# Kernel optimization log

Hardware: AMD Instinct MI355X
Metric: run time of the kernel (lower is better)

The kernel has to match this reference:

```python
import jax, jax.numpy as jnp
import numpy as np

B, T, D, H, HD, L, V = 2048, 64, 128, 4, 32, 6, 256
DFF = 4 * D
PARAM_NAMES = ['tok_emb', 'pos_emb', 'Wq', 'Wk', 'Wv', 'Wo', 'bo', 'ln1_g', 'ln1_b',
               'W1', 'b1', 'W2', 'b2', 'ln2_g', 'ln2_b', 'lnf_g', 'lnf_b', 'Wh', 'bh']


def setup_inputs() -> dict:
    key = jax.random.key(0)
    ks = jax.random.split(key, 12)
    def n(k, shape, s=0.02):
        return jax.random.normal(k, shape, jnp.float32) * s
    return dict(
        idx=jax.random.randint(ks[0], (B, T), 0, V),
        tok_emb=n(ks[1], (V, D)),
        pos_emb=n(ks[2], (T, D)),
        Wq=n(ks[3], (L, H, D, HD)),
        Wk=n(ks[4], (L, H, D, HD)),
        Wv=n(ks[5], (L, H, D, HD)),
        Wo=n(ks[6], (L, D, D)), bo=jnp.zeros((L, D), jnp.float32),
        ln1_g=jnp.ones((L, D), jnp.float32), ln1_b=jnp.zeros((L, D), jnp.float32),
        W1=n(ks[7], (L, D, DFF)), b1=jnp.zeros((L, DFF), jnp.float32),
        W2=n(ks[8], (L, DFF, D)), b2=jnp.zeros((L, D), jnp.float32),
        ln2_g=jnp.ones((L, D), jnp.float32), ln2_b=jnp.zeros((L, D), jnp.float32),
        lnf_g=jnp.ones((D,), jnp.float32), lnf_b=jnp.zeros((D,), jnp.float32),
        Wh=n(ks[9], (D, V)), bh=jnp.zeros((V,), jnp.float32),
    )


def _ln(x, g, b):
    m = x.mean(-1, keepdims=True)
    v = x.var(-1, keepdims=True)  # biased, matches torch LayerNorm
    return (x - m) / jnp.sqrt(v + 1e-5) * g + b


def _forward(idx, p):
    x = p['tok_emb'][idx] + p['pos_emb'][None, :, :]  # [B,T,D]
    mask = jnp.tril(jnp.ones((T, T), bool))

    def block(x, lp):
        Wq, Wk, Wv, Wo, bo, g1, bb1, W1, b1, W2, b2, g2, bb2 = lp
        h = _ln(x, g1, bb1)
        q = jnp.einsum('btd,hde->bhte', h, Wq)
        k = jnp.einsum('btd,hde->bhte', h, Wk)
        v = jnp.einsum('btd,hde->bhte', h, Wv)
        s = jnp.einsum('bhte,bhse->bhts', q, k) * (HD ** -0.5)
        s = jnp.where(mask, s, -jnp.inf)
        w = jax.nn.softmax(s, axis=-1)  # dropout inactive (eval mode)
        o = jnp.einsum('bhts,bhse->bthe', w, v).reshape(B, T, D)  # concat heads
        x = x + o @ Wo + bo
        h2 = _ln(x, g2, bb2)
        x = x + jax.nn.relu(h2 @ W1 + b1) @ W2 + b2
        return x, None

    lp = (p['Wq'], p['Wk'], p['Wv'], p['Wo'], p['bo'], p['ln1_g'], p['ln1_b'],
          p['W1'], p['b1'], p['W2'], p['b2'], p['ln2_g'], p['ln2_b'])
    x, _ = jax.lax.scan(block, x, lp)
    x = _ln(x, p['lnf_g'], p['lnf_b'])
    return x @ p['Wh'] + p['bh']  # [B,T,V] logits


def reference(idx, tok_emb, pos_emb, Wq, Wk, Wv, Wo, bo, ln1_g, ln1_b,
              W1, b1, W2, b2, ln2_g, ln2_b, lnf_g, lnf_b, Wh, bh):
    p = dict(zip(PARAM_NAMES, (tok_emb, pos_emb, Wq, Wk, Wv, Wo, bo, ln1_g, ln1_b,
                               W1, b1, W2, b2, ln2_g, ln2_b, lnf_g, lnf_b, Wh, bh)))
    return _forward(idx, p)
```

## Files before the change

kernel.cpp:

```cpp
#include <hip/hip_runtime.h>

typedef unsigned short ushort_t;
typedef __attribute__((ext_vector_type(8))) short short8;
typedef __attribute__((ext_vector_type(4))) float float4_;

#define B_   2048
#define T_   64
#define D_   128
#define H_   4
#define HD_  32
#define L_   6
#define V_   256
#define DFF_ 512
#define BT_  (B_*T_)

static __device__ __forceinline__ float b2f(ushort_t u) {
    return __uint_as_float(((unsigned int)u) << 16);
}
static __device__ __forceinline__ ushort_t f2b(float f) {
    unsigned int x = __float_as_uint(f);
    return (ushort_t)((x + 0x7fffu + ((x >> 16) & 1u)) >> 16);
}
static __device__ __forceinline__ int bf16_mode(const ushort_t* flag_src) {
    return flag_src[0] == 0x3F80;
}

#define AS1C(p) ((const __attribute__((address_space(1))) void*)(p))
#define AS3(p)  ((__attribute__((address_space(3))) void*)(p))

#define NCVT 19
struct Cvt {
    const void* src[NCVT];
    long base[NCVT];
    long total;
};

__global__ __launch_bounds__(256) void convert_all(
    Cvt c, ushort_t* __restrict__ dst, const ushort_t* __restrict__ flag_src)
{
    long i = (long)blockIdx.x * 256 + threadIdx.x;
    if (i >= c.total) return;
    int s = 0;
    #pragma unroll 1
    while (s + 1 < NCVT && i >= c.base[s + 1]) s++;
    long j = i - c.base[s];
    if (bf16_mode(flag_src))
        dst[i] = ((const ushort_t*)c.src[s])[j];
    else
        dst[i] = f2b(((const float*)c.src[s])[j]);
}

__global__ __launch_bounds__(256) void repack_qkv(
    const ushort_t* __restrict__ Wq, const ushort_t* __restrict__ Wk,
    const ushort_t* __restrict__ Wv, ushort_t* __restrict__ outw)
{
    int i = blockIdx.x * 256 + threadIdx.x;
    int d = i & 127;
    int c = (i >> 7) % 384;
    int l = i / (384 * 128);
    int sel = c >> 7, hh = (c >> 5) & 3, e = c & 31;
    const ushort_t* W = (sel == 0) ? Wq : (sel == 1) ? Wk : Wv;
    outw[i] = W[((l * 4 + hh) * 128 + d) * 32 + e];
}

__global__ __launch_bounds__(256) void transpose_w(
    const ushort_t* __restrict__ in, ushort_t* __restrict__ out, int K, int N)
{
    long i = (long)blockIdx.x * 256 + threadIdx.x;
    int n = (int)(i % N);
    int k = (int)((i / N) % K);
    int l = (int)(i / ((long)N * K));
    out[((long)l * N + n) * K + k] = in[i];
}

__global__ __launch_bounds__(256) void embed_ln_kernel(
    const int* __restrict__ idx, const ushort_t* __restrict__ tok,
    const ushort_t* __restrict__ pos, const ushort_t* __restrict__ g,
    const ushort_t* __restrict__ bta, float* __restrict__ x,
    ushort_t* __restrict__ hout)
{
    int row  = blockIdx.x * 4 + (threadIdx.x >> 6);
    int lane = threadIdx.x & 63;
    int t = row & 63;
    int id = idx[row];
    float v0 = b2f(tok[id * 128 + lane])      + b2f(pos[t * 128 + lane]);
    float v1 = b2f(tok[id * 128 + lane + 64]) + b2f(pos[t * 128 + lane + 64]);
    long o = (long)row * 128 + lane;
    x[o] = v0; x[o + 64] = v1;
    float s  = v0 + v1;
    float sq = v0 * v0 + v1 * v1;
    #pragma unroll
    for (int off = 1; off < 64; off <<= 1) {
        s  += __shfl_xor(s,  off);
        sq += __shfl_xor(sq, off);
    }
    float mean = s * (1.0f / 128.0f);
    float var  = sq * (1.0f / 128.0f) - mean * mean;
    float rstd = rsqrtf(var + 1e-5f);
    hout[o]      = f2b((v0 - mean) * rstd * b2f(g[lane])      + b2f(bta[lane]));
    hout[o + 64] = f2b((v1 - mean) * rstd * b2f(g[lane + 64]) + b2f(bta[lane + 64]));
}

__global__ __launch_bounds__(256) void gemm_bt(
    const ushort_t* __restrict__ A, const ushort_t* __restrict__ Bt,
    const ushort_t* __restrict__ bias, void* __restrict__ outp,
    const ushort_t* __restrict__ flag, int M, int N, int K, int relu)
{
    __shared__ __align__(16) ushort_t As[128 * 64];
    __shared__ __align__(16) ushort_t Bs[128 * 64];
    const int tid  = threadIdx.x;
    const int wave = tid >> 6, lane = tid & 63;
    const int wm = wave >> 1, wn = wave & 1;
    const int row0 = blockIdx.x * 128, col0 = blockIdx.y * 128;

    float4_ acc[4][4];
    #pragma unroll
    for (int m = 0; m < 4; m++)
        #pragma unroll
        for (int n = 0; n < 4; n++) acc[m][n] = (float4_)0.0f;

    const int srow = lane >> 3;
    const int scg  = (lane & 7) ^ srow;
    const int fr = lane & 15, fq = lane >> 4;

    for (int k0 = 0; k0 < K; k0 += 64) {
        __syncthreads();
        #pragma unroll
        for (int i = 0; i < 4; i++) {
            int chunk = wave * 4 + i;
            int r = chunk * 8 + srow;
            __builtin_amdgcn_global_load_lds(
                AS1C(&A[(size_t)(row0 + r) * K + k0 + scg * 8]),
                AS3(&As[chunk * 512]), 16, 0, 0);
            __builtin_amdgcn_global_load_lds(
                AS1C(&Bt[(size_t)(col0 + r) * K + k0 + scg * 8]),
                AS3(&Bs[chunk * 512]), 16, 0, 0);
        }
        __syncthreads();

        #pragma unroll
        for (int ks = 0; ks < 2; ks++) {
            short8 af[4], bf[4];
            #pragma unroll
            for (int mt = 0; mt < 4; mt++) {
                int r = wm * 64 + mt * 16 + fr;
                af[mt] = *(const short8*)&As[r * 64 + (((ks * 4 + fq) ^ (r & 7)) * 8)];
            }
            #pragma unroll
            for (int nt = 0; nt < 4; nt++) {
                int r = wn * 64 + nt * 16 + fr;
                bf[nt] = *(const short8*)&Bs[r * 64 + (((ks * 4 + fq) ^ (r & 7)) * 8)];
            }
            #pragma unroll
            for (int mt = 0; mt < 4; mt++)
                #pragma unroll
                for (int nt = 0; nt < 4; nt++)
                    acc[mt][nt] = __builtin_amdgcn_mfma_f32_16x16x32_bf16(
                        af[mt], bf[nt], acc[mt][nt], 0, 0, 0);
        }
    }

    const int out_bf16 = (flag == nullptr) || bf16_mode(flag);
    #pragma unroll
    for (int nt = 0; nt < 4; nt++) {
        int gcol = col0 + wn * 64 + nt * 16 + fr;
        float bb = bias ? b2f(bias[gcol]) : 0.0f;
        #pragma unroll
        for (int mt = 0; mt < 4; mt++) {
            #pragma unroll
            for (int i = 0; i < 4; i++) {
                int grow = row0 + wm * 64 + mt * 16 + fq * 4 + i;
                float v = acc[mt][nt][i] + bb;
                if (relu) v = fmaxf(v, 0.0f);
                long off = (long)grow * N + gcol;
                if (out_bf16) ((ushort_t*)outp)[off] = f2b(v);
                else          ((float*)outp)[off] = v;
            }
        }
    }
}

__global__ __launch_bounds__(256) void gemm_ln(
    const ushort_t* __restrict__ A, const ushort_t* __restrict__ Bt,
    const ushort_t* __restrict__ bias, float* __restrict__ x,
    const ushort_t* __restrict__ g, const ushort_t* __restrict__ bta,
    ushort_t* __restrict__ hout, int M, int K)
{
    __shared__ __align__(16) ushort_t As[128 * 64];
    __shared__ __align__(16) ushort_t Bs[128 * 64];
    __shared__ float stats[128][2][2];
    const int tid  = threadIdx.x;
    const int wave = tid >> 6, lane = tid & 63;
    const int wm = wave >> 1, wn = wave & 1;
    const int row0 = blockIdx.x * 128;
    const int N = 128;

    float4_ acc[4][4];
    #pragma unroll
    for (int m = 0; m < 4; m++)
        #pragma unroll
        for (int n = 0; n < 4; n++) acc[m][n] = (float4_)0.0f;

    const int srow = lane >> 3;
    const int scg  = (lane & 7) ^ srow;
    const int fr = lane & 15, fq = lane >> 4;

    for (int k0 = 0; k0 < K; k0 += 64) {
        __syncthreads();
        #pragma unroll
        for (int i = 0; i < 4; i++) {
            int chunk = wave * 4 + i;
            int r = chunk * 8 + srow;
            __builtin_amdgcn_global_load_lds(
                AS1C(&A[(size_t)(row0 + r) * K + k0 + scg * 8]),
                AS3(&As[chunk * 512]), 16, 0, 0);
            __builtin_amdgcn_global_load_lds(
                AS1C(&Bt[(size_t)r * K + k0 + scg * 8]),
                AS3(&Bs[chunk * 512]), 16, 0, 0);
        }
        __syncthreads();

        #pragma unroll
        for (int ks = 0; ks < 2; ks++) {
            short8 af[4], bf[4];
            #pragma unroll
            for (int mt = 0; mt < 4; mt++) {
                int r = wm * 64 + mt * 16 + fr;
                af[mt] = *(const short8*)&As[r * 64 + (((ks * 4 + fq) ^ (r & 7)) * 8)];
            }
            #pragma unroll
            for (int nt = 0; nt < 4; nt++) {
                int r = wn * 64 + nt * 16 + fr;
                bf[nt] = *(const short8*)&Bs[r * 64 + (((ks * 4 + fq) ^ (r & 7)) * 8)];
            }
            #pragma unroll
            for (int mt = 0; mt < 4; mt++)
                #pragma unroll
                for (int nt = 0; nt < 4; nt++)
                    acc[mt][nt] = __builtin_amdgcn_mfma_f32_16x16x32_bf16(
                        af[mt], bf[nt], acc[mt][nt], 0, 0, 0);
        }
    }

    int   col[4];
    float bbias[4], gg[4], bln[4];
    #pragma unroll
    for (int nt = 0; nt < 4; nt++) {
        col[nt]  = wn * 64 + nt * 16 + fr;
        bbias[nt] = b2f(bias[col[nt]]);
        gg[nt]    = b2f(g[col[nt]]);
        bln[nt]   = b2f(bta[col[nt]]);
    }
    #pragma unroll
    for (int mt = 0; mt < 4; mt++) {
        #pragma unroll
        for (int i = 0; i < 4; i++) {
            int lr = wm * 64 + mt * 16 + fq * 4 + i;
            long rbase = (long)(row0 + lr) * N;
            float s = 0.0f, sq = 0.0f;
            #pragma unroll
            for (int nt = 0; nt < 4; nt++) {
                float nx = x[rbase + col[nt]] + acc[mt][nt][i] + bbias[nt];
                x[rbase + col[nt]] = nx;
                acc[mt][nt][i] = nx;
                s += nx; sq += nx * nx;
            }
            s  += __shfl_xor(s, 1);  sq += __shfl_xor(sq, 1);
            s  += __shfl_xor(s, 2);  sq += __shfl_xor(sq, 2);
            s  += __shfl_xor(s, 4);  sq += __shfl_xor(sq, 4);
            s  += __shfl_xor(s, 8);  sq += __shfl_xor(sq, 8);
            if (fr == 0) { stats[lr][wn][0] = s; stats[lr][wn][1] = sq; }
        }
    }
    __syncthreads();
    #pragma unroll
    for (int mt = 0; mt < 4; mt++) {
        #pragma unroll
        for (int i = 0; i < 4; i++) {
            int lr = wm * 64 + mt * 16 + fq * 4 + i;
            float s  = stats[lr][0][0] + stats[lr][1][0];
            float sq = stats[lr][0][1] + stats[lr][1][1];
            float mean = s * (1.0f / 128.0f);
            float var  = sq * (1.0f / 128.0f) - mean * mean;
            float rstd = rsqrtf(var + 1e-5f);
            long rbase = (long)(row0 + lr) * N;
            #pragma unroll
            for (int nt = 0; nt < 4; nt++) {
                float nx = acc[mt][nt][i];
                hout[rbase + col[nt]] = f2b((nx - mean) * rstd * gg[nt] + bln[nt]);
            }
        }
    }
}

__global__ __launch_bounds__(256) void ffn_fused(
    const ushort_t* __restrict__ hin,
    const ushort_t* __restrict__ w1,
    const ushort_t* __restrict__ b1v,
    const ushort_t* __restrict__ w2,
    const ushort_t* __restrict__ b2v,
    float* __restrict__ x,
    const ushort_t* __restrict__ g, const ushort_t* __restrict__ bta,
    ushort_t* __restrict__ hout)
{
    __shared__ __align__(16) ushort_t Hs[64 * 128];
    __shared__ __align__(16) ushort_t Ms[64 * 128];
    __shared__ __align__(16) ushort_t Bs[128 * 64];
    __shared__ float stats[64][2][2];
    const int tid  = threadIdx.x;
    const int wave = tid >> 6, lane = tid & 63;
    const int wm = wave >> 1, wn = wave & 1;
    const int row0 = blockIdx.x * 64;

    const int srow = lane >> 3;
    const int scg  = (lane & 7) ^ srow;
    const int fr = lane & 15, fq = lane >> 4;

    {
        int lr4 = lane >> 4, pg = lane & 15;
        #pragma unroll
        for (int i = 0; i < 4; i++) {
            int c = wave * 4 + i;
            int r = c * 4 + lr4;
            int kg = pg ^ (r & 7);
            __builtin_amdgcn_global_load_lds(
                AS1C(&hin[(size_t)(row0 + r) * 128 + kg * 8]),
                AS3(&Hs[c * 512]), 16, 0, 0);
        }
    }

    float4_ acc2[2][4];
    #pragma unroll
    for (int m = 0; m < 2; m++)
        #pragma unroll
        for (int n = 0; n < 4; n++) acc2[m][n] = (float4_)0.0f;

    #pragma unroll 1
    for (int c = 0; c < 4; c++) {
        const ushort_t* Wc = w1 + (size_t)c * 128 * 128;
        float4_ acc1[2][4];
        #pragma unroll
        for (int m = 0; m < 2; m++)
            #pragma unroll
            for (int n = 0; n < 4; n++) acc1[m][n] = (float4_)0.0f;

        #pragma unroll 1
        for (int k0 = 0; k0 < 128; k0 += 64) {
            __syncthreads();
            #pragma unroll
            for (int i = 0; i < 4; i++) {
                int chunk = wave * 4 + i;
                int r = chunk * 8 + srow;
                __builtin_amdgcn_global_load_lds(
                    AS1C(&Wc[(size_t)r * 128 + k0 + scg * 8]),
                    AS3(&Bs[chunk * 512]), 16, 0, 0);
            }
            __syncthreads();
            #pragma unroll
            for (int ks = 0; ks < 2; ks++) {
                int kb = (k0 >> 5) + ks;
                short8 af[2], bf[4];
                #pragma unroll
                for (int mt = 0; mt < 2; mt++) {
                    int r = wm * 32 + mt * 16 + fr;
                    af[mt] = *(const short8*)&Hs[r * 128 + (((kb * 4 + fq) ^ (r & 7)) * 8)];
                }
                #pragma unroll
                for (int nt = 0; nt < 4; nt++) {
                    int r = wn * 64 + nt * 16 + fr;
                    bf[nt] = *(const short8*)&Bs[r * 64 + (((ks * 4 + fq) ^ (r & 7)) * 8)];
                }
                #pragma unroll
                for (int mt = 0; mt < 2; mt++)
                    #pragma unroll
                    for (int nt = 0; nt < 4; nt++)
                        acc1[mt][nt] = __builtin_amdgcn_mfma_f32_16x16x32_bf16(
                            af[mt], bf[nt], acc1[mt][nt], 0, 0, 0);
            }
        }

        #pragma unroll
        for (int nt = 0; nt < 4; nt++) {
            int col = wn * 64 + nt * 16 + fr;
            float bb = b2f(b1v[c * 128 + col]);
            #pragma unroll
            for (int mt = 0; mt < 2; mt++) {
                #pragma unroll
                for (int i = 0; i < 4; i++) {
                    int row = wm * 32 + mt * 16 + fq * 4 + i;
                    float v = fmaxf(acc1[mt][nt][i] + bb, 0.0f);
                    Ms[row * 128 + (((col >> 3) ^ (row & 7)) * 8) + (col & 7)] = f2b(v);
                }
            }
        }

        #pragma unroll 1
        for (int k0 = 0; k0 < 128; k0 += 64) {
            __syncthreads();
            #pragma unroll
            for (int i = 0; i < 4; i++) {
                int chunk = wave * 4 + i;
                int r = chunk * 8 + srow;
                __builtin_amdgcn_global_load_lds(
                    AS1C(&w2[(size_t)r * 512 + c * 128 + k0 + scg * 8]),
                    AS3(&Bs[chunk * 512]), 16, 0, 0);
            }
            __syncthreads();
            #pragma unroll
            for (int ks = 0; ks < 2; ks++) {
                int kb = (k0 >> 5) + ks;
                short8 af[2], bf[4];
                #pragma unroll
                for (int mt = 0; mt < 2; mt++) {
                    int r = wm * 32 + mt * 16 + fr;
                    af[mt] = *(const short8*)&Ms[r * 128 + (((kb * 4 + fq) ^ (r & 7)) * 8)];
                }
                #pragma unroll
                for (int nt = 0; nt < 4; nt++) {
                    int r = wn * 64 + nt * 16 + fr;
                    bf[nt] = *(const short8*)&Bs[r * 64 + (((ks * 4 + fq) ^ (r & 7)) * 8)];
                }
                #pragma unroll
                for (int mt = 0; mt < 2; mt++)
                    #pragma unroll
                    for (int nt = 0; nt < 4; nt++)
                        acc2[mt][nt] = __builtin_amdgcn_mfma_f32_16x16x32_bf16(
                            af[mt], bf[nt], acc2[mt][nt], 0, 0, 0);
            }
        }
    }

    int   col[4];
    float bbias[4], gg[4], bln[4];
    #pragma unroll
    for (int nt = 0; nt < 4; nt++) {
        col[nt]  = wn * 64 + nt * 16 + fr;
        bbias[nt] = b2f(b2v[col[nt]]);
        gg[nt]    = b2f(g[col[nt]]);
        bln[nt]   = b2f(bta[col[nt]]);
    }
    #pragma unroll
    for (int mt = 0; mt < 2; mt++) {
        #pragma unroll
        for (int i = 0; i < 4; i++) {
            int lr = wm * 32 + mt * 16 + fq * 4 + i;
            long rbase = (long)(row0 + lr) * 128;
            float s = 0.0f, sq = 0.0f;
            #pragma unroll
            for (int nt = 0; nt < 4; nt++) {
                float nx = x[rbase + col[nt]] + acc2[mt][nt][i] + bbias[nt];
                x[rbase + col[nt]] = nx;
                acc2[mt][nt][i] = nx;
                s += nx; sq += nx * nx;
            }
            s  += __shfl_xor(s, 1);  sq += __shfl_xor(sq, 1);
            s  += __shfl_xor(s, 2);  sq += __shfl_xor(sq, 2);
            s  += __shfl_xor(s, 4);  sq += __shfl_xor(sq, 4);
            s  += __shfl_xor(s, 8);  sq += __shfl_xor(sq, 8);
            if (fr == 0) { stats[lr][wn][0] = s; stats[lr][wn][1] = sq; }
        }
    }
    __syncthreads();
    #pragma unroll
    for (int mt = 0; mt < 2; mt++) {
        #pragma unroll
        for (int i = 0; i < 4; i++) {
            int lr = wm * 32 + mt * 16 + fq * 4 + i;
            float s  = stats[lr][0][0] + stats[lr][1][0];
            float sq = stats[lr][0][1] + stats[lr][1][1];
            float mean = s * (1.0f / 128.0f);
            float var  = sq * (1.0f / 128.0f) - mean * mean;
            float rstd = rsqrtf(var + 1e-5f);
            long rbase = (long)(row0 + lr) * 128;
            #pragma unroll
            for (int nt = 0; nt < 4; nt++) {
                float nx = acc2[mt][nt][i];
                hout[rbase + col[nt]] = f2b((nx - mean) * rstd * gg[nt] + bln[nt]);
            }
        }
    }
}

__global__ __launch_bounds__(256) void attn_kernel(
    const ushort_t* __restrict__ qkv,
    ushort_t* __restrict__ out)
{
    __shared__ __align__(16) ushort_t Qs[64][40];
    __shared__ __align__(16) ushort_t Ks[64][40];
    __shared__ __align__(16) ushort_t Vt[32][72];
    __shared__ __align__(16) ushort_t Pb[64][72];
    const int tid = threadIdx.x;
    const int b = blockIdx.x >> 2, h = blockIdx.x & 3;
    const long base = (long)b * T_ * 384 + h * 32;

    {
        int t = tid >> 2, e8 = (tid & 3) * 8;
        const ushort_t* p = &qkv[base + (long)t * 384 + e8];
        short8 qv = *(const short8*)(p);
        short8 kv = *(const short8*)(p + 128);
        short8 vv = *(const short8*)(p + 256);
        *(short8*)&Qs[t][e8] = qv;
        *(short8*)&Ks[t][e8] = kv;
        #pragma unroll
        for (int j = 0; j < 8; j++) Vt[e8 + j][t] = (ushort_t)vv[j];
    }
    __syncthreads();

    const int w = tid >> 6, lane = tid & 63, fr = lane & 15, fq = lane >> 4;

    short8 qf = *(const short8*)&Qs[w * 16 + fr][fq * 8];
    float4_ s[4];
    #pragma unroll
    for (int tj = 0; tj < 4; tj++) s[tj] = (float4_)0.0f;
    #pragma unroll
    for (int tj = 0; tj < 4; tj++) {
        if (tj <= w) {
            short8 kf = *(const short8*)&Ks[tj * 16 + fr][fq * 8];
            s[tj] = __builtin_amdgcn_mfma_f32_16x16x32_bf16(qf, kf, s[tj], 0, 0, 0);
        }
    }

    const float scale = 0.17677669529663687f;
    float pv[4][4];
    #pragma unroll
    for (int i = 0; i < 4; i++) {
        float mx = -1.0e30f;
        float vv4[4];
        int   ok[4];
        #pragma unroll
        for (int tj = 0; tj < 4; tj++) {
            ok[tj] = (tj < w) || (tj == w && fr <= fq * 4 + i);
            float v = ok[tj] ? s[tj][i] * scale : -1.0e30f;
            vv4[tj] = v;
            mx = fmaxf(mx, v);
        }
        mx = fmaxf(mx, __shfl_xor(mx, 1));
        mx = fmaxf(mx, __shfl_xor(mx, 2));
        mx = fmaxf(mx, __shfl_xor(mx, 4));
        mx = fmaxf(mx, __shfl_xor(mx, 8));
        float sm = 0.0f;
        #pragma unroll
        for (int tj = 0; tj < 4; tj++) {
            float e = ok[tj] ? __expf(vv4[tj] - mx) : 0.0f;
            vv4[tj] = e;
            sm += e;
        }
        sm += __shfl_xor(sm, 1);
        sm += __shfl_xor(sm, 2);
        sm += __shfl_xor(sm, 4);
        sm += __shfl_xor(sm, 8);
        float inv = 1.0f / sm;
        #pragma unroll
        for (int tj = 0; tj < 4; tj++) pv[i][tj] = vv4[tj] * inv;
    }
    #pragma unroll
    for (int tj = 0; tj < 4; tj++)
        #pragma unroll
        for (int i = 0; i < 4; i++)
            Pb[w * 16 + fq * 4 + i][tj * 16 + fr] = f2b(pv[i][tj]);
    __syncthreads();

    float4_ o[2];
    o[0] = (float4_)0.0f; o[1] = (float4_)0.0f;
    #pragma unroll
    for (int ks = 0; ks < 2; ks++) {
        short8 pf = *(const short8*)&Pb[w * 16 + fr][ks * 32 + fq * 8];
        #pragma unroll
        for (int nt = 0; nt < 2; nt++) {
            short8 vf = *(const short8*)&Vt[nt * 16 + fr][ks * 32 + fq * 8];
            o[nt] = __builtin_amdgcn_mfma_f32_16x16x32_bf16(pf, vf, o[nt], 0, 0, 0);
        }
    }
    #pragma unroll
    for (int nt = 0; nt < 2; nt++)
        #pragma unroll
        for (int i = 0; i < 4; i++)
            out[(long)(b * T_ + w * 16 + fq * 4 + i) * 128 + h * 32 + nt * 16 + fr]
                = f2b(o[nt][i]);
}

extern "C" void kernel_launch(void* const* d_in, const int* in_sizes, int n_in,
                              void* d_out, int out_size, void* d_ws, size_t ws_size,
                              hipStream_t stream)
{
    (void)in_sizes; (void)n_in; (void)out_size; (void)ws_size;
    const int* idx = (const int*)d_in[0];
    const ushort_t* flag = (const ushort_t*)d_in[8];

    char* ws = (char*)d_ws;
    float*    x    = (float*)ws;     ws += (size_t)BT_ * D_ * 4;
    ushort_t* h    = (ushort_t*)ws;  ws += (size_t)BT_ * D_ * 2;
    ushort_t* qkvb = (ushort_t*)ws;  ws += (size_t)BT_ * 384 * 2;
    ushort_t* ao   = (ushort_t*)ws;  ws += (size_t)BT_ * D_ * 2;
    ushort_t* wqkv = (ushort_t*)ws;  ws += (size_t)L_ * 384 * 128 * 2;
    ushort_t* wo   = (ushort_t*)ws;  ws += (size_t)L_ * 128 * 128 * 2;
    ushort_t* w1   = (ushort_t*)ws;  ws += (size_t)L_ * 512 * 128 * 2;
    ushort_t* w2   = (ushort_t*)ws;  ws += (size_t)L_ * 128 * 512 * 2;
    ushort_t* wh   = (ushort_t*)ws;  ws += (size_t)256 * 128 * 2;
    ushort_t* cvt  = (ushort_t*)ws;

    static const long cnt[NCVT] = {
        (long)V_*D_, (long)T_*D_,
        (long)L_*H_*D_*HD_, (long)L_*H_*D_*HD_, (long)L_*H_*D_*HD_,
        (long)L_*D_*D_, (long)L_*D_,
        (long)L_*D_, (long)L_*D_,
        (long)L_*D_*DFF_, (long)L_*DFF_,
        (long)L_*DFF_*D_, (long)L_*D_,
        (long)L_*D_, (long)L_*D_,
        (long)D_, (long)D_,
        (long)D_*V_, (long)V_
    };
    Cvt c;
    long off = 0;
    for (int i = 0; i < NCVT; i++) { c.src[i] = d_in[i + 1]; c.base[i] = off; off += cnt[i]; }
    c.total = off;
    ushort_t* ctok  = cvt + c.base[0];
    ushort_t* cpos  = cvt + c.base[1];
    ushort_t* cWq   = cvt + c.base[2];
    ushort_t* cWk   = cvt + c.base[3];
    ushort_t* cWv   = cvt + c.base[4];
    ushort_t* cWo   = cvt + c.base[5];
    ushort_t* cbo   = cvt + c.base[6];
    ushort_t* cln1g = cvt + c.base[7];
    ushort_t* cln1b = cvt + c.base[8];
    ushort_t* cW1   = cvt + c.base[9];
    ushort_t* cb1   = cvt + c.base[10];
    ushort_t* cW2   = cvt + c.base[11];
    ushort_t* cb2   = cvt + c.base[12];
    ushort_t* cln2g = cvt + c.base[13];
    ushort_t* cln2b = cvt + c.base[14];
    ushort_t* clnfg = cvt + c.base[15];
    ushort_t* clnfb = cvt + c.base[16];
    ushort_t* cWh   = cvt + c.base[17];
    ushort_t* cbh   = cvt + c.base[18];

    convert_all<<<(int)((c.total + 255) / 256), 256, 0, stream>>>(c, cvt, flag);

    repack_qkv <<<1152, 256, 0, stream>>>(cWq, cWk, cWv, wqkv);
    transpose_w<<<384,  256, 0, stream>>>(cWo, wo, 128, 128);
    transpose_w<<<1536, 256, 0, stream>>>(cW1, w1, 128, 512);
    transpose_w<<<1536, 256, 0, stream>>>(cW2, w2, 512, 128);
    transpose_w<<<128,  256, 0, stream>>>(cWh, wh, 128, 256);
    embed_ln_kernel<<<BT_ / 4, 256, 0, stream>>>(idx, ctok, cpos, cln1g, cln1b, x, h);

    for (int l = 0; l < L_; l++) {
        gemm_bt<<<dim3(BT_ / 128, 3), 256, 0, stream>>>(
            h, wqkv + l * 384 * 128, nullptr, qkvb, nullptr, BT_, 384, 128, 0);
        attn_kernel<<<B_ * H_, 256, 0, stream>>>(qkvb, ao);
        gemm_ln<<<BT_ / 128, 256, 0, stream>>>(
            ao, wo + l * 128 * 128, cbo + l * 128, x,
            cln2g + l * 128, cln2b + l * 128, h, BT_, 128);
        const ushort_t* ng = (l < L_ - 1) ? (cln1g + (l + 1) * 128) : clnfg;
        const ushort_t* nb = (l < L_ - 1) ? (cln1b + (l + 1) * 128) : clnfb;
        ffn_fused<<<BT_ / 64, 256, 0, stream>>>(
            h, w1 + l * 512 * 128, cb1 + l * 512,
            w2 + l * 128 * 512, cb2 + l * 128, x, ng, nb, h);
    }
    gemm_bt<<<dim3(BT_ / 128, 2), 256, 0, stream>>>(
        h, wh, cbh, d_out, flag, BT_, 256, 128, 0);
}
```

Baseline: 1.509 ms.

## Fuse QKV projection into attention kernel per batch-head block

Removes the separate QKV GEMM and its intermediate qkv buffer. Each attention block loads the 64x128 hidden tile into LDS with a swizzled async global-to-LDS load and computes its head's Q, K and V with MFMA directly. Weight fragments are read straight from global memory. This eliminates the write and re-read of the qkv activation, but each batch's hidden tile is now loaded four times (once per head). It also adds extra LDS usage that may reduce occupancy.

```diff
diff --git a/kernel.cpp b/kernel.cpp
--- a/kernel.cpp
+++ b/kernel.cpp
@@ -481,32 +481,72 @@
     }
 }
 
-__global__ __launch_bounds__(256) void attn_kernel(
-    const ushort_t* __restrict__ qkv,
+__global__ __launch_bounds__(256) void attn_qkv(
+    const ushort_t* __restrict__ hin,
+    const ushort_t* __restrict__ wqkv,
     ushort_t* __restrict__ out)
 {
+    __shared__ __align__(16) ushort_t Hb[64 * 128];
     __shared__ __align__(16) ushort_t Qs[64][40];
     __shared__ __align__(16) ushort_t Ks[64][40];
     __shared__ __align__(16) ushort_t Vt[32][72];
     __shared__ __align__(16) ushort_t Pb[64][72];
     const int tid = threadIdx.x;
     const int b = blockIdx.x >> 2, h = blockIdx.x & 3;
-    const long base = (long)b * T_ * 384 + h * 32;
+    const int w = tid >> 6, lane = tid & 63;
+    const int fr = lane & 15, fq = lane >> 4;
+    const long rowg0 = (long)b * 64;
 
     {
-        int t = tid >> 2, e8 = (tid & 3) * 8;
-        const ushort_t* p = &qkv[base + (long)t * 384 + e8];
-        short8 qv = *(const short8*)(p);
-        short8 kv = *(const short8*)(p + 128);
-        short8 vv = *(const short8*)(p + 256);
-        *(short8*)&Qs[t][e8] = qv;
-        *(short8*)&Ks[t][e8] = kv;
-        #pragma unroll
-        for (int j = 0; j < 8; j++) Vt[e8 + j][t] = (ushort_t)vv[j];
+        int lr4 = lane >> 4, pg = lane & 15;
+        #pragma unroll
+        for (int i = 0; i < 4; i++) {
+            int c = w * 4 + i;
+            int r = c * 4 + lr4;
+            int kg = pg ^ (r & 7);
+            __builtin_amdgcn_global_load_lds(
+                AS1C(&hin[(rowg0 + r) * 128 + kg * 8]),
+                AS3(&Hb[c * 512]), 16, 0, 0);
+        }
     }
     __syncthreads();
 
-    const int w = tid >> 6, lane = tid & 63, fr = lane & 15, fq = lane >> 4;
+    {
+        short8 af[4];
+        #pragma unroll
+        for (int kb = 0; kb < 4; kb++) {
+            int r = w * 16 + fr;
+            af[kb] = *(const short8*)&Hb[r * 128 + (((kb * 4 + fq) ^ (r & 7)) * 8)];
+        }
+        float4_ aq[2], ak[2], av[2];
+        #pragma unroll
+        for (int nt = 0; nt < 2; nt++) {
+            aq[nt] = (float4_)0.0f; ak[nt] = (float4_)0.0f; av[nt] = (float4_)0.0f;
+        }
+        #pragma unroll
+        for (int kb = 0; kb < 4; kb++) {
+            #pragma unroll
+            for (int nt = 0; nt < 2; nt++) {
+                int colq = h * 32 + nt * 16 + fr;
+                short8 bq = *(const short8*)&wqkv[(size_t)colq * 128 + kb * 32 + fq * 8];
+                short8 bk = *(const short8*)&wqkv[(size_t)(colq + 128) * 128 + kb * 32 + fq * 8];
+                short8 bv = *(const short8*)&wqkv[(size_t)(colq + 256) * 128 + kb * 32 + fq * 8];
+                aq[nt] = __builtin_amdgcn_mfma_f32_16x16x32_bf16(af[kb], bq, aq[nt], 0, 0, 0);
+                ak[nt] = __builtin_amdgcn_mfma_f32_16x16x32_bf16(af[kb], bk, ak[nt], 0, 0, 0);
+                av[nt] = __builtin_amdgcn_mfma_f32_16x16x32_bf16(af[kb], bv, av[nt], 0, 0, 0);
+            }
+        }
+        #pragma unroll
+        for (int nt = 0; nt < 2; nt++)
+            #pragma unroll
+            for (int i = 0; i < 4; i++) {
+                int t = w * 16 + fq * 4 + i, e = nt * 16 + fr;
+                Qs[t][e] = f2b(aq[nt][i]);
+                Ks[t][e] = f2b(ak[nt][i]);
+                Vt[e][t] = f2b(av[nt][i]);
+            }
+    }
+    __syncthreads();
 
     short8 qf = *(const short8*)&Qs[w * 16 + fr][fq * 8];
     float4_ s[4];
@@ -575,7 +615,7 @@
     for (int nt = 0; nt < 2; nt++)
         #pragma unroll
         for (int i = 0; i < 4; i++)
-            out[(long)(b * T_ + w * 16 + fq * 4 + i) * 128 + h * 32 + nt * 16 + fr]
+            out[(rowg0 + w * 16 + fq * 4 + i) * 128 + h * 32 + nt * 16 + fr]
                 = f2b(o[nt][i]);
 }
 
@@ -590,7 +630,6 @@
     char* ws = (char*)d_ws;
     float*    x    = (float*)ws;     ws += (size_t)BT_ * D_ * 4;
     ushort_t* h    = (ushort_t*)ws;  ws += (size_t)BT_ * D_ * 2;
-    ushort_t* qkvb = (ushort_t*)ws;  ws += (size_t)BT_ * 384 * 2;
     ushort_t* ao   = (ushort_t*)ws;  ws += (size_t)BT_ * D_ * 2;
     ushort_t* wqkv = (ushort_t*)ws;  ws += (size_t)L_ * 384 * 128 * 2;
     ushort_t* wo   = (ushort_t*)ws;  ws += (size_t)L_ * 128 * 128 * 2;
@@ -644,9 +683,7 @@
     embed_ln_kernel<<<BT_ / 4, 256, 0, stream>>>(idx, ctok, cpos, cln1g, cln1b, x, h);
 
     for (int l = 0; l < L_; l++) {
-        gemm_bt<<<dim3(BT_ / 128, 3), 256, 0, stream>>>(
-            h, wqkv + l * 384 * 128, nullptr, qkvb, nullptr, BT_, 384, 128, 0);
-        attn_kernel<<<B_ * H_, 256, 0, stream>>>(qkvb, ao);
+        attn_qkv<<<B_ * H_, 256, 0, stream>>>(h, wqkv + l * 384 * 128, ao);
         gemm_ln<<<BT_ / 128, 256, 0, stream>>>(
             ao, wo + l * 128 * 128, cbo + l * 128, x,
             cln2g + l * 128, cln2b + l * 128, h, BT_, 128);
```

Result: slower. 1.612 ms (+6.8%).

## Fuse attention output projection and LN2 into the FFN kernel

Applied to the files above, without the earlier changes.

Merges the out-projection GEMM with its residual-add and LayerNorm into the fused FFN kernel, so the normalized activations stay in LDS instead of being written to and reread from global memory. This removes one kernel launch per layer and one bf16 round-trip of h, but the fused kernel uses 64-row tiles for the projection instead of 128 and reuses the attention-input LDS buffer for the FFN hidden tile.

```diff
diff --git a/kernel.cpp b/kernel.cpp
--- a/kernel.cpp
+++ b/kernel.cpp
@@ -180,307 +180,6 @@
     }
 }
 
-__global__ __launch_bounds__(256) void gemm_ln(
-    const ushort_t* __restrict__ A, const ushort_t* __restrict__ Bt,
-    const ushort_t* __restrict__ bias, float* __restrict__ x,
-    const ushort_t* __restrict__ g, const ushort_t* __restrict__ bta,
-    ushort_t* __restrict__ hout, int M, int K)
-{
-    __shared__ __align__(16) ushort_t As[128 * 64];
-    __shared__ __align__(16) ushort_t Bs[128 * 64];
-    __shared__ float stats[128][2][2];
-    const int tid  = threadIdx.x;
-    const int wave = tid >> 6, lane = tid & 63;
-    const int wm = wave >> 1, wn = wave & 1;
-    const int row0 = blockIdx.x * 128;
-    const int N = 128;
-
-    float4_ acc[4][4];
-    #pragma unroll
-    for (int m = 0; m < 4; m++)
-        #pragma unroll
-        for (int n = 0; n < 4; n++) acc[m][n] = (float4_)0.0f;
-
-    const int srow = lane >> 3;
-    const int scg  = (lane & 7) ^ srow;
-    const int fr = lane & 15, fq = lane >> 4;
-
-    for (int k0 = 0; k0 < K; k0 += 64) {
-        __syncthreads();
-        #pragma unroll
-        for (int i = 0; i < 4; i++) {
-            int chunk = wave * 4 + i;
-            int r = chunk * 8 + srow;
-            __builtin_amdgcn_global_load_lds(
-                AS1C(&A[(size_t)(row0 + r) * K + k0 + scg * 8]),
-                AS3(&As[chunk * 512]), 16, 0, 0);
-            __builtin_amdgcn_global_load_lds(
-                AS1C(&Bt[(size_t)r * K + k0 + scg * 8]),
-                AS3(&Bs[chunk * 512]), 16, 0, 0);
-        }
-        __syncthreads();
-
-        #pragma unroll
-        for (int ks = 0; ks < 2; ks++) {
-            short8 af[4], bf[4];
-            #pragma unroll
-            for (int mt = 0; mt < 4; mt++) {
-                int r = wm * 64 + mt * 16 + fr;
-                af[mt] = *(const short8*)&As[r * 64 + (((ks * 4 + fq) ^ (r & 7)) * 8)];
-            }
-            #pragma unroll
-            for (int nt = 0; nt < 4; nt++) {
-                int r = wn * 64 + nt * 16 + fr;
-                bf[nt] = *(const short8*)&Bs[r * 64 + (((ks * 4 + fq) ^ (r & 7)) * 8)];
-            }
-            #pragma unroll
-            for (int mt = 0; mt < 4; mt++)
-                #pragma unroll
-                for (int nt = 0; nt < 4; nt++)
-                    acc[mt][nt] = __builtin_amdgcn_mfma_f32_16x16x32_bf16(
-                        af[mt], bf[nt], acc[mt][nt], 0, 0, 0);
-        }
-    }
-
-    int   col[4];
-    float bbias[4], gg[4], bln[4];
-    #pragma unroll
-    for (int nt = 0; nt < 4; nt++) {
-        col[nt]  = wn * 64 + nt * 16 + fr;
-        bbias[nt] = b2f(bias[col[nt]]);
-        gg[nt]    = b2f(g[col[nt]]);
-        bln[nt]   = b2f(bta[col[nt]]);
-    }
-    #pragma unroll
-    for (int mt = 0; mt < 4; mt++) {
-        #pragma unroll
-        for (int i = 0; i < 4; i++) {
-            int lr = wm * 64 + mt * 16 + fq * 4 + i;
-            long rbase = (long)(row0 + lr) * N;
-            float s = 0.0f, sq = 0.0f;
-            #pragma unroll
-            for (int nt = 0; nt < 4; nt++) {
-                float nx = x[rbase + col[nt]] + acc[mt][nt][i] + bbias[nt];
-                x[rbase + col[nt]] = nx;
-                acc[mt][nt][i] = nx;
-                s += nx; sq += nx * nx;
-            }
-            s  += __shfl_xor(s, 1);  sq += __shfl_xor(sq, 1);
-            s  += __shfl_xor(s, 2);  sq += __shfl_xor(sq, 2);
-            s  += __shfl_xor(s, 4);  sq += __shfl_xor(sq, 4);
-            s  += __shfl_xor(s, 8);  sq += __shfl_xor(sq, 8);
-            if (fr == 0) { stats[lr][wn][0] = s; stats[lr][wn][1] = sq; }
-        }
-    }
-    __syncthreads();
-    #pragma unroll
-    for (int mt = 0; mt < 4; mt++) {
-        #pragma unroll
-        for (int i = 0; i < 4; i++) {
-            int lr = wm * 64 + mt * 16 + fq * 4 + i;
-            float s  = stats[lr][0][0] + stats[lr][1][0];
-            float sq = stats[lr][0][1] + stats[lr][1][1];
-            float mean = s * (1.0f / 128.0f);
-            float var  = sq * (1.0f / 128.0f) - mean * mean;
-            float rstd = rsqrtf(var + 1e-5f);
-            long rbase = (long)(row0 + lr) * N;
-            #pragma unroll
-            for (int nt = 0; nt < 4; nt++) {
-                float nx = acc[mt][nt][i];
-                hout[rbase + col[nt]] = f2b((nx - mean) * rstd * gg[nt] + bln[nt]);
-            }
-        }
-    }
-}
-
-__global__ __launch_bounds__(256) void ffn_fused(
-    const ushort_t* __restrict__ hin,
-    const ushort_t* __restrict__ w1,
-    const ushort_t* __restrict__ b1v,
-    const ushort_t* __restrict__ w2,
-    const ushort_t* __restrict__ b2v,
-    float* __restrict__ x,
-    const ushort_t* __restrict__ g, const ushort_t* __restrict__ bta,
-    ushort_t* __restrict__ hout)
-{
-    __shared__ __align__(16) ushort_t Hs[64 * 128];
-    __shared__ __align__(16) ushort_t Ms[64 * 128];
-    __shared__ __align__(16) ushort_t Bs[128 * 64];
-    __shared__ float stats[64][2][2];
-    const int tid  = threadIdx.x;
-    const int wave = tid >> 6, lane = tid & 63;
-    const int wm = wave >> 1, wn = wave & 1;
-    const int row0 = blockIdx.x * 64;
-
-    const int srow = lane >> 3;
-    const int scg  = (lane & 7) ^ srow;
-    const int fr = lane & 15, fq = lane >> 4;
-
-    {
-        int lr4 = lane >> 4, pg = lane & 15;
-        #pragma unroll
-        for (int i = 0; i < 4; i++) {
-            int c = wave * 4 + i;
-            int r = c * 4 + lr4;
-            int kg = pg ^ (r & 7);
-            __builtin_amdgcn_global_load_lds(
-                AS1C(&hin[(size_t)(row0 + r) * 128 + kg * 8]),
-                AS3(&Hs[c * 512]), 16, 0, 0);
-        }
-    }
-
-    float4_ acc2[2][4];
-    #pragma unroll
-    for (int m = 0; m < 2; m++)
-        #pragma unroll
-        for (int n = 0; n < 4; n++) acc2[m][n] = (float4_)0.0f;
-
-    #pragma unroll 1
-    for (int c = 0; c < 4; c++) {
-        const ushort_t* Wc = w1 + (size_t)c * 128 * 128;
-        float4_ acc1[2][4];
-        #pragma unroll
-        for (int m = 0; m < 2; m++)
-            #pragma unroll
-            for (int n = 0; n < 4; n++) acc1[m][n] = (float4_)0.0f;
-
-        #pragma unroll 1
-        for (int k0 = 0; k0 < 128; k0 += 64) {
-            __syncthreads();
-            #pragma unroll
-            for (int i = 0; i < 4; i++) {
-                int chunk = wave * 4 + i;
-                int r = chunk * 8 + srow;
-                __builtin_amdgcn_global_load_lds(
-                    AS1C(&Wc[(size_t)r * 128 + k0 + scg * 8]),
-                    AS3(&Bs[chunk * 512]), 16, 0, 0);
-            }
-            __syncthreads();
-            #pragma unroll
-            for (int ks = 0; ks < 2; ks++) {
-                int kb = (k0 >> 5) + ks;
-                short8 af[2], bf[4];
-                #pragma unroll
-                for (int mt = 0; mt < 2; mt++) {
-                    int r = wm * 32 + mt * 16 + fr;
-                    af[mt] = *(const short8*)&Hs[r * 128 + (((kb * 4 + fq) ^ (r & 7)) * 8)];
-                }
-                #pragma unroll
-                for (int nt = 0; nt < 4; nt++) {
-                    int r = wn * 64 + nt * 16 + fr;
-                    bf[nt] = *(const short8*)&Bs[r * 64 + (((ks * 4 + fq) ^ (r & 7)) * 8)];
-                }
-                #pragma unroll
-                for (int mt = 0; mt < 2; mt++)
-                    #pragma unroll
-                    for (int nt = 0; nt < 4; nt++)
-                        acc1[mt][nt] = __builtin_amdgcn_mfma_f32_16x16x32_bf16(
-                            af[mt], bf[nt], acc1[mt][nt], 0, 0, 0);
-            }
-        }
-
-        #pragma unroll
-        for (int nt = 0; nt < 4; nt++) {
-            int col = wn * 64 + nt * 16 + fr;
-            float bb = b2f(b1v[c * 128 + col]);
-            #pragma unroll
-            for (int mt = 0; mt < 2; mt++) {
-                #pragma unroll
-                for (int i = 0; i < 4; i++) {
-                    int row = wm * 32 + mt * 16 + fq * 4 + i;
-                    float v = fmaxf(acc1[mt][nt][i] + bb, 0.0f);
-                    Ms[row * 128 + (((col >> 3) ^ (row & 7)) * 8) + (col & 7)] = f2b(v);
-                }
-            }
-        }
-
-        #pragma unroll 1
-        for (int k0 = 0; k0 < 128; k0 += 64) {
-            __syncthreads();
-            #pragma unroll
-            for (int i = 0; i < 4; i++) {
-                int chunk = wave * 4 + i;
-                int r = chunk * 8 + srow;
-                __builtin_amdgcn_global_load_lds(
-                    AS1C(&w2[(size_t)r * 512 + c * 128 + k0 + scg * 8]),
-                    AS3(&Bs[chunk * 512]), 16, 0, 0);
-            }
-            __syncthreads();
-            #pragma unroll
-            for (int ks = 0; ks < 2; ks++) {
-                int kb = (k0 >> 5) + ks;
-                short8 af[2], bf[4];
-                #pragma unroll
-                for (int mt = 0; mt < 2; mt++) {
-                    int r = wm * 32 + mt * 16 + fr;
-                    af[mt] = *(const short8*)&Ms[r * 128 + (((kb * 4 + fq) ^ (r & 7)) * 8)];
-                }
-                #pragma unroll
-                for (int nt = 0; nt < 4; nt++) {
-                    int r = wn * 64 + nt * 16 + fr;
-                    bf[nt] = *(const short8*)&Bs[r * 64 + (((ks * 4 + fq) ^ (r & 7)) * 8)];
-                }
-                #pragma unroll
-                for (int mt = 0; mt < 2; mt++)
-                    #pragma unroll
-                    for (int nt = 0; nt < 4; nt++)
-                        acc2[mt][nt] = __builtin_amdgcn_mfma_f32_16x16x32_bf16(
-                            af[mt], bf[nt], acc2[mt][nt], 0, 0, 0);
-            }
-        }
-    }
-
-    int   col[4];
-    float bbias[4], gg[4], bln[4];
-    #pragma unroll
-    for (int nt = 0; nt < 4; nt++) {
-        col[nt]  = wn * 64 + nt * 16 + fr;
-        bbias[nt] = b2f(b2v[col[nt]]);
-        gg[nt]    = b2f(g[col[nt]]);
-        bln[nt]   = b2f(bta[col[nt]]);
-    }
-    #pragma unroll
-    for (int mt = 0; mt < 2; mt++) {
-        #pragma unroll
-        for (int i = 0; i < 4; i++) {
-            int lr = wm * 32 + mt * 16 + fq * 4 + i;
-            long rbase = (long)(row0 + lr) * 128;
-            float s = 0.0f, sq = 0.0f;
-            #pragma unroll
-            for (int nt = 0; nt < 4; nt++) {
-                float nx = x[rbase + col[nt]] + acc2[mt][nt][i] + bbias[nt];
-                x[rbase + col[nt]] = nx;
-                acc2[mt][nt][i] = nx;
-                s += nx; sq += nx * nx;
-            }
-            s  += __shfl_xor(s, 1);  sq += __shfl_xor(sq, 1);
-            s  += __shfl_xor(s, 2);  sq += __shfl_xor(sq, 2);
-            s  += __shfl_xor(s, 4);  sq += __shfl_xor(sq, 4);
-            s  += __shfl_xor(s, 8);  sq += __shfl_xor(sq, 8);
-            if (fr == 0) { stats[lr][wn][0] = s; stats[lr][wn][1] = sq; }
-        }
-    }
-    __syncthreads();
-    #pragma unroll
-    for (int mt = 0; mt < 2; mt++) {
-        #pragma unroll
-        for (int i = 0; i < 4; i++) {
-            int lr = wm * 32 + mt * 16 + fq * 4 + i;
-            float s  = stats[lr][0][0] + stats[lr][1][0];
-            float sq = stats[lr][0][1] + stats[lr][1][1];
-            float mean = s * (1.0f / 128.0f);
-            float var  = sq * (1.0f / 128.0f) - mean * mean;
-            float rstd = rsqrtf(var + 1e-5f);
-            long rbase = (long)(row0 + lr) * 128;
-            #pragma unroll
-            for (int nt = 0; nt < 4; nt++) {
-                float nx = acc2[mt][nt][i];
-                hout[rbase + col[nt]] = f2b((nx - mean) * rstd * gg[nt] + bln[nt]);
-            }
-        }
-    }
-}
-
 __global__ __launch_bounds__(256) void attn_kernel(
     const ushort_t* __restrict__ qkv,
     ushort_t* __restrict__ out)
@@ -577,6 +276,291 @@
         for (int i = 0; i < 4; i++)
             out[(long)(b * T_ + w * 16 + fq * 4 + i) * 128 + h * 32 + nt * 16 + fr]
                 = f2b(o[nt][i]);
+}
+
+__global__ __launch_bounds__(256) void proj_ffn(
+    const ushort_t* __restrict__ ao,
+    const ushort_t* __restrict__ wo,
+    const ushort_t* __restrict__ bov,
+    const ushort_t* __restrict__ g2, const ushort_t* __restrict__ b2ln,
+    const ushort_t* __restrict__ w1,
+    const ushort_t* __restrict__ b1v,
+    const ushort_t* __restrict__ w2,
+    const ushort_t* __restrict__ b2v,
+    float* __restrict__ x,
+    const ushort_t* __restrict__ gn, const ushort_t* __restrict__ bn,
+    ushort_t* __restrict__ hout)
+{
+    __shared__ __align__(16) ushort_t AsMs[64 * 128];
+    __shared__ __align__(16) ushort_t Hs[64 * 128];
+    __shared__ __align__(16) ushort_t Bs[128 * 64];
+    __shared__ float stats[64][2][2];
+    const int tid  = threadIdx.x;
+    const int wave = tid >> 6, lane = tid & 63;
+    const int wm = wave >> 1, wn = wave & 1;
+    const int row0 = blockIdx.x * 64;
+    const int srow = lane >> 3;
+    const int scg  = (lane & 7) ^ srow;
+    const int fr = lane & 15, fq = lane >> 4;
+
+    {
+        int lr4 = lane >> 4, pg = lane & 15;
+        #pragma unroll
+        for (int i = 0; i < 4; i++) {
+            int c = wave * 4 + i;
+            int r = c * 4 + lr4;
+            int kg = pg ^ (r & 7);
+            __builtin_amdgcn_global_load_lds(
+                AS1C(&ao[(size_t)(row0 + r) * 128 + kg * 8]),
+                AS3(&AsMs[c * 512]), 16, 0, 0);
+        }
+    }
+
+    float4_ accp[2][4];
+    #pragma unroll
+    for (int m = 0; m < 2; m++)
+        #pragma unroll
+        for (int n = 0; n < 4; n++) accp[m][n] = (float4_)0.0f;
+
+    #pragma unroll 1
+    for (int k0 = 0; k0 < 128; k0 += 64) {
+        __syncthreads();
+        #pragma unroll
+        for (int i = 0; i < 4; i++) {
+            int chunk = wave * 4 + i;
+            int r = chunk * 8 + srow;
+            __builtin_amdgcn_global_load_lds(
+                AS1C(&wo[(size_t)r * 128 + k0 + scg * 8]),
+                AS3(&Bs[chunk * 512]), 16, 0, 0);
+        }
+        __syncthreads();
+        #pragma unroll
+        for (int ks = 0; ks < 2; ks++) {
+            int kb = (k0 >> 5) + ks;
+            short8 af[2], bf[4];
+            #pragma unroll
+            for (int mt = 0; mt < 2; mt++) {
+                int r = wm * 32 + mt * 16 + fr;
+                af[mt] = *(const short8*)&AsMs[r * 128 + (((kb * 4 + fq) ^ (r & 7)) * 8)];
+            }
+            #pragma unroll
+            for (int nt = 0; nt < 4; nt++) {
+                int r = wn * 64 + nt * 16 + fr;
+                bf[nt] = *(const short8*)&Bs[r * 64 + (((ks * 4 + fq) ^ (r & 7)) * 8)];
+            }
+            #pragma unroll
+            for (int mt = 0; mt < 2; mt++)
+                #pragma unroll
+                for (int nt = 0; nt < 4; nt++)
+                    accp[mt][nt] = __builtin_amdgcn_mfma_f32_16x16x32_bf16(
+                        af[mt], bf[nt], accp[mt][nt], 0, 0, 0);
+        }
+    }
+
+    int   col[4];
+    {
+        float bb[4], gg[4], bl[4];
+        #pragma unroll
+        for (int nt = 0; nt < 4; nt++) {
+            col[nt] = wn * 64 + nt * 16 + fr;
+            bb[nt] = b2f(bov[col[nt]]);
+            gg[nt] = b2f(g2[col[nt]]);
+            bl[nt] = b2f(b2ln[col[nt]]);
+        }
+        #pragma unroll
+        for (int mt = 0; mt < 2; mt++) {
+            #pragma unroll
+            for (int i = 0; i < 4; i++) {
+                int lr = wm * 32 + mt * 16 + fq * 4 + i;
+                long rbase = (long)(row0 + lr) * 128;
+                float s = 0.0f, sq = 0.0f;
+                #pragma unroll
+                for (int nt = 0; nt < 4; nt++) {
+                    float nx = x[rbase + col[nt]] + accp[mt][nt][i] + bb[nt];
+                    x[rbase + col[nt]] = nx;
+                    accp[mt][nt][i] = nx;
+                    s += nx; sq += nx * nx;
+                }
+                s  += __shfl_xor(s, 1);  sq += __shfl_xor(sq, 1);
+                s  += __shfl_xor(s, 2);  sq += __shfl_xor(sq, 2);
+                s  += __shfl_xor(s, 4);  sq += __shfl_xor(sq, 4);
+                s  += __shfl_xor(s, 8);  sq += __shfl_xor(sq, 8);
+                if (fr == 0) { stats[lr][wn][0] = s; stats[lr][wn][1] = sq; }
+            }
+        }
+        __syncthreads();
+        #pragma unroll
+        for (int mt = 0; mt < 2; mt++) {
+            #pragma unroll
+            for (int i = 0; i < 4; i++) {
+                int lr = wm * 32 + mt * 16 + fq * 4 + i;
+                float s  = stats[lr][0][0] + stats[lr][1][0];
+                float sq = stats[lr][0][1] + stats[lr][1][1];
+                float mean = s * (1.0f / 128.0f);
+                float var  = sq * (1.0f / 128.0f) - mean * mean;
+                float rstd = rsqrtf(var + 1e-5f);
+                #pragma unroll
+                for (int nt = 0; nt < 4; nt++) {
+                    float nx = accp[mt][nt][i];
+                    int cv = col[nt];
+                    Hs[lr * 128 + (((cv >> 3) ^ (lr & 7)) * 8) + (cv & 7)]
+                        = f2b((nx - mean) * rstd * gg[nt] + bl[nt]);
+                }
+            }
+        }
+    }
+
+    float4_ acc2[2][4];
+    #pragma unroll
+    for (int m = 0; m < 2; m++)
+        #pragma unroll
+        for (int n = 0; n < 4; n++) acc2[m][n] = (float4_)0.0f;
+
+    #pragma unroll 1
+    for (int c = 0; c < 4; c++) {
+        const ushort_t* Wc = w1 + (size_t)c * 128 * 128;
+        float4_ acc1[2][4];
+        #pragma unroll
+        for (int m = 0; m < 2; m++)
+            #pragma unroll
+            for (int n = 0; n < 4; n++) acc1[m][n] = (float4_)0.0f;
+
+        #pragma unroll 1
+        for (int k0 = 0; k0 < 128; k0 += 64) {
+            __syncthreads();
+            #pragma unroll
+            for (int i = 0; i < 4; i++) {
+                int chunk = wave * 4 + i;
+                int r = chunk * 8 + srow;
+                __builtin_amdgcn_global_load_lds(
+                    AS1C(&Wc[(size_t)r * 128 + k0 + scg * 8]),
+                    AS3(&Bs[chunk * 512]), 16, 0, 0);
+            }
+            __syncthreads();
+            #pragma unroll
+            for (int ks = 0; ks < 2; ks++) {
+                int kb = (k0 >> 5) + ks;
+                short8 af[2], bf[4];
+                #pragma unroll
+                for (int mt = 0; mt < 2; mt++) {
+                    int r = wm * 32 + mt * 16 + fr;
+                    af[mt] = *(const short8*)&Hs[r * 128 + (((kb * 4 + fq) ^ (r & 7)) * 8)];
+                }
+                #pragma unroll
+                for (int nt = 0; nt < 4; nt++) {
+                    int r = wn * 64 + nt * 16 + fr;
+                    bf[nt] = *(const short8*)&Bs[r * 64 + (((ks * 4 + fq) ^ (r & 7)) * 8)];
+                }
+                #pragma unroll
+                for (int mt = 0; mt < 2; mt++)
+                    #pragma unroll
+                    for (int nt = 0; nt < 4; nt++)
+                        acc1[mt][nt] = __builtin_amdgcn_mfma_f32_16x16x32_bf16(
+                            af[mt], bf[nt], acc1[mt][nt], 0, 0, 0);
+            }
+        }
+
+        #pragma unroll
+        for (int nt = 0; nt < 4; nt++) {
+            int cv = wn * 64 + nt * 16 + fr;
+            float bbm = b2f(b1v[c * 128 + cv]);
+            #pragma unroll
+            for (int mt = 0; mt < 2; mt++) {
+                #pragma unroll
+                for (int i = 0; i < 4; i++) {
+                    int row = wm * 32 + mt * 16 + fq * 4 + i;
+                    float v = fmaxf(acc1[mt][nt][i] + bbm, 0.0f);
+                    AsMs[row * 128 + (((cv >> 3) ^ (row & 7)) * 8) + (cv & 7)] = f2b(v);
+                }
+            }
+        }
+
+        #pragma unroll 1
+        for (int k0 = 0; k0 < 128; k0 += 64) {
+            __syncthreads();
+            #pragma unroll
+            for (int i = 0; i < 4; i++) {
+                int chunk = wave * 4 + i;
+                int r = chunk * 8 + srow;
+                __builtin_amdgcn_global_load_lds(
+                    AS1C(&w2[(size_t)r * 512 + c * 128 + k0 + scg * 8]),
+                    AS3(&Bs[chunk * 512]), 16, 0, 0);
+            }
+            __syncthreads();
+            #pragma unroll
+            for (int ks = 0; ks < 2; ks++) {
+                int kb = (k0 >> 5) + ks;
+                short8 af[2], bf[4];
+                #pragma unroll
+                for (int mt = 0; mt < 2; mt++) {
+                    int r = wm * 32 + mt * 16 + fr;
+                    af[mt] = *(const short8*)&AsMs[r * 128 + (((kb * 4 + fq) ^ (r & 7)) * 8)];
+                }
+                #pragma unroll
+                for (int nt = 0; nt < 4; nt++) {
+                    int r = wn * 64 + nt * 16 + fr;
+                    bf[nt] = *(const short8*)&Bs[r * 64 + (((ks * 4 + fq) ^ (r & 7)) * 8)];
+                }
+                #pragma unroll
+                for (int mt = 0; mt < 2; mt++)
+                    #pragma unroll
+                    for (int nt = 0; nt < 4; nt++)
+                        acc2[mt][nt] = __builtin_amdgcn_mfma_f32_16x16x32_bf16(
+                            af[mt], bf[nt], acc2[mt][nt], 0, 0, 0);
+            }
+        }
+    }
+
+    __syncthreads();
+    {
+        float bb[4], gg[4], bl[4];
+        #pragma unroll
+        for (int nt = 0; nt < 4; nt++) {
+            bb[nt] = b2f(b2v[col[nt]]);
+            gg[nt] = b2f(gn[col[nt]]);
+            bl[nt] = b2f(bn[col[nt]]);
+        }
+        #pragma unroll
+        for (int mt = 0; mt < 2; mt++) {
+            #pragma unroll
+            for (int i = 0; i < 4; i++) {
+                int lr = wm * 32 + mt * 16 + fq * 4 + i;
+                long rbase = (long)(row0 + lr) * 128;
+                float s = 0.0f, sq = 0.0f;
+                #pragma unroll
+                for (int nt = 0; nt < 4; nt++) {
+                    float nx = x[rbase + col[nt]] + acc2[mt][nt][i] + bb[nt];
+                    x[rbase + col[nt]] = nx;
+                    acc2[mt][nt][i] = nx;
+                    s += nx; sq += nx * nx;
+                }
+                s  += __shfl_xor(s, 1);  sq += __shfl_xor(sq, 1);
+                s  += __shfl_xor(s, 2);  sq += __shfl_xor(sq, 2);
+                s  += __shfl_xor(s, 4);  sq += __shfl_xor(sq, 4);
+                s  += __shfl_xor(s, 8);  sq += __shfl_xor(sq, 8);
+                if (fr == 0) { stats[lr][wn][0] = s; stats[lr][wn][1] = sq; }
+            }
+        }
+        __syncthreads();
+        #pragma unroll
+        for (int mt = 0; mt < 2; mt++) {
+            #pragma unroll
+            for (int i = 0; i < 4; i++) {
+                int lr = wm * 32 + mt * 16 + fq * 4 + i;
+                float s  = stats[lr][0][0] + stats[lr][1][0];
+                float sq = stats[lr][0][1] + stats[lr][1][1];
+                float mean = s * (1.0f / 128.0f);
+                float var  = sq * (1.0f / 128.0f) - mean * mean;
+                float rstd = rsqrtf(var + 1e-5f);
+                long rbase = (long)(row0 + lr) * 128;
+                #pragma unroll
+                for (int nt = 0; nt < 4; nt++) {
+                    float nx = acc2[mt][nt][i];
+                    hout[rbase + col[nt]] = f2b((nx - mean) * rstd * gg[nt] + bl[nt]);
+                }
+            }
+        }
+    }
 }
 
 extern "C" void kernel_launch(void* const* d_in, const int* in_sizes, int n_in,
@@ -647,14 +631,14 @@
         gemm_bt<<<dim3(BT_ / 128, 3), 256, 0, stream>>>(
             h, wqkv + l * 384 * 128, nullptr, qkvb, nullptr, BT_, 384, 128, 0);
         attn_kernel<<<B_ * H_, 256, 0, stream>>>(qkvb, ao);
-        gemm_ln<<<BT_ / 128, 256, 0, stream>>>(
-            ao, wo + l * 128 * 128, cbo + l * 128, x,
-            cln2g + l * 128, cln2b + l * 128, h, BT_, 128);
         const ushort_t* ng = (l < L_ - 1) ? (cln1g + (l + 1) * 128) : clnfg;
         const ushort_t* nb = (l < L_ - 1) ? (cln1b + (l + 1) * 128) : clnfb;
-        ffn_fused<<<BT_ / 64, 256, 0, stream>>>(
-            h, w1 + l * 512 * 128, cb1 + l * 512,
-            w2 + l * 128 * 512, cb2 + l * 128, x, ng, nb, h);
+        proj_ffn<<<BT_ / 64, 256, 0, stream>>>(
+            ao, wo + l * 128 * 128, cbo + l * 128,
+            cln2g + l * 128, cln2b + l * 128,
+            w1 + l * 512 * 128, cb1 + l * 512,
+            w2 + l * 128 * 512, cb2 + l * 128,
+            x, ng, nb, h);
     }
     gemm_bt<<<dim3(BT_ / 128, 2), 256, 0, stream>>>(
         h, wh, cbh, d_out, flag, BT_, 256, 128, 0);
```

After: 1.443 ms (median of 2 runs). 4.4% less time.
